# Optimization experiments

Measured on AMD Instinct MI355X. Metric: run time of the kernel, lower is better.

## Reference

```python
import jax, jax.numpy as jnp
import numpy as np

N_HEAD = 16
N_EMBD = 2048
B, S = 2, 2048


def setup_inputs() -> dict:
    key = jax.random.key(0)
    k1, k2, k3 = jax.random.split(key, 3)
    scale = 0.02
    return {
        "hidden_states": jax.random.normal(k1, (B, S, N_EMBD), dtype=jnp.float32),
        "attention_mask": jnp.ones((B, S), dtype=jnp.float32),
        "w_attn": jax.random.normal(k2, (N_EMBD, 3 * N_EMBD), dtype=jnp.float32) * scale,
        "b_attn": jnp.zeros((3 * N_EMBD,), dtype=jnp.float32),
        "w_proj": jax.random.normal(k3, (N_EMBD, N_EMBD), dtype=jnp.float32) * scale,
        "b_proj": jnp.zeros((N_EMBD,), dtype=jnp.float32),
    }


def reference(hidden_states, attention_mask, w_attn, b_attn, w_proj, b_proj):
    b, s, d = hidden_states.shape
    h = N_HEAD
    dh = d // h
    qkv = hidden_states @ w_attn + b_attn          # [b, s, 3d]
    q, k, v = jnp.split(qkv, 3, axis=-1)
    # [b, s, d] -> [b, h, s, dh]
    q = q.reshape(b, s, h, dh).transpose(0, 2, 1, 3)
    k = k.reshape(b, s, h, dh).transpose(0, 2, 1, 3)
    v = v.reshape(b, s, h, dh).transpose(0, 2, 1, 3)
    scores = jnp.einsum("bhqd,bhkd->bhqk", q, k) / jnp.sqrt(jnp.float32(dh))
    # padding mask: [b, s] -> additive bias [b, 1, 1, s]
    bias = (1.0 - attention_mask)[:, None, None, :] * -10000.0
    attn = jax.nn.softmax(scores + bias, axis=-1)   # dropout p=0 (eval)
    out = jnp.einsum("bhqk,bhkd->bhqd", attn, v)    # [b, h, s, dh]
    out = out.transpose(0, 2, 1, 3).reshape(b, s, d)
    return out @ w_proj + b_proj
```

## Files before the change

kernel.cpp:

```cpp
#include <hip/hip_runtime.h>
#include <stdint.h>

#define B_   2
#define S_   2048
#define D_   2048
#define NH_  16
#define DH_  128
#define N3_  6144

typedef unsigned short u16;
typedef __bf16 bf16x8 __attribute__((ext_vector_type(8)));
typedef float  f32x4  __attribute__((ext_vector_type(4)));

#define QSCALE   (0.08838834764831845f * 1.4426950408889634f)
#define BIASF    (-10000.0f * 1.4426950408889634f)

__device__ __forceinline__ u16 f2bf(float f) {
  union { float f; unsigned u; } v; v.f = f;
  unsigned u = v.u;
  return (u16)((u + 0x7FFFu + ((u >> 16) & 1u)) >> 16);
}

__device__ __forceinline__ float fast_exp2(float x) {
  float r;
  asm("v_exp_f32 %0, %1" : "=v"(r) : "v"(x));
  return r;
}

__device__ __forceinline__ unsigned cvtpk(float lo, float hi) {
  unsigned r;
  asm("v_cvt_pk_bf16_f32 %0, %1, %2" : "=v"(r) : "v"(lo), "v"(hi));
  return r;
}

#define GL2LDS(gsrc, ldst)                                                              \
  __builtin_amdgcn_global_load_lds((const __attribute__((address_space(1))) void*)(gsrc), \
      (__attribute__((address_space(3))) void*)(ldst), 16, 0, 0)

__device__ __forceinline__ int swz_id() {
  int id = blockIdx.y * gridDim.x + blockIdx.x;
  int cpx = (gridDim.x * gridDim.y) >> 3;
  return (id & 7) * cpx + (id >> 3);
}

__global__ void cvt_kernel(const float* __restrict__ in, u16* __restrict__ out, int n4) {
  int i = blockIdx.x * blockDim.x + threadIdx.x;
  int stride = gridDim.x * blockDim.x;
  for (; i < n4; i += stride) {
    float4 v = ((const float4*)in)[i];
    ushort4 o;
    o.x = f2bf(v.x); o.y = f2bf(v.y); o.z = f2bf(v.z); o.w = f2bf(v.w);
    ((ushort4*)out)[i] = o;
  }
}

__global__ void transpose_kernel(const float* __restrict__ in, u16* __restrict__ out,
                                 int K, int N) {
  __shared__ float tile[32][33];
  int tx = threadIdx.x, ty = threadIdx.y;
  int nx = blockIdx.x * 32, ky = blockIdx.y * 32;
#pragma unroll
  for (int j = 0; j < 32; j += 8)
    tile[ty + j][tx] = in[(size_t)(ky + ty + j) * N + nx + tx];
  __syncthreads();
#pragma unroll
  for (int j = 0; j < 32; j += 8)
    out[(size_t)(nx + ty + j) * K + ky + tx] = f2bf(tile[tx][ty + j]);
}


#define KS_ABASE(c, h) (lds + (c) * 24576 + (h) * 8192)
#define KS_BBASE(c, h) (lds + (c) * 24576 + 16384 + (h) * 4096)
#define VMCNT(n) asm volatile("s_waitcnt vmcnt(" #n ")" ::: "memory")
#define LGKM0                                            \
  do {                                                   \
    asm volatile("s_waitcnt lgkmcnt(0)" ::: "memory");   \
    __builtin_amdgcn_sched_barrier(0);                   \
  } while (0)
#define BAR __builtin_amdgcn_s_barrier()

__device__ __forceinline__ void ks_read_set(const u16* __restrict__ Ab,
                                            const u16* __restrict__ Bb,
                                            int wrB, int wcB, int lr, int g,
                                            bf16x8 (&af)[4], bf16x8 (&bf)[4]) {
#pragma unroll
  for (int i = 0; i < 4; ++i) {
    int r = wrB + i * 16 + lr;
    int pr = r >> 1;
    int slot = (((r & 1) << 2) | g) ^ (pr & 7);
    af[i] = *reinterpret_cast<const bf16x8*>(Ab + pr * 64 + slot * 8);
  }
#pragma unroll
  for (int j = 0; j < 4; ++j) {
    int n = wcB + j * 16 + lr;
    int pn = n >> 1;
    int slot = (((n & 1) << 2) | g) ^ (pn & 7);
    bf[j] = *reinterpret_cast<const bf16x8*>(Bb + pn * 64 + slot * 8);
  }
}

__device__ __forceinline__ void ks_mfma(const bf16x8 (&af)[4], const bf16x8 (&bf)[4],
                                        f32x4 (&acc)[4][4]) {
  __builtin_amdgcn_s_setprio(1);
#pragma unroll
  for (int i = 0; i < 4; ++i)
#pragma unroll
    for (int j = 0; j < 4; ++j)
      acc[i][j] = __builtin_amdgcn_mfma_f32_16x16x32_bf16(af[i], bf[j], acc[i][j], 0, 0, 0);
  __builtin_amdgcn_s_setprio(0);
}

template <int KD>
__device__ __forceinline__ void ks_stage(const u16* __restrict__ A,
                                         const u16* __restrict__ BT, u16* lds,
                                         int c, int h, int Tg, int m0, int n0, int t) {
#pragma unroll
  for (int inst = 0; inst < 2; ++inst) {
    int idx = inst * 512 + t;
    int pr = idx >> 3, s = idx & 7, v = s ^ (pr & 7);
    int r = pr * 2 + (v >> 2), g = v & 3;
    GL2LDS(A + (size_t)(m0 + r) * KD + Tg * 64 + h * 32 + g * 8,
           KS_ABASE(c, h) + idx * 8);
  }
  {
    int idx = t;
    int pn = idx >> 3, s = idx & 7, v = s ^ (pn & 7);
    int n = pn * 2 + (v >> 2), g = v & 3;
    GL2LDS(BT + (size_t)(n0 + n) * KD + Tg * 64 + h * 32 + g * 8,
           KS_BBASE(c, h) + idx * 8);
  }
}

template <int KD>
__device__ __forceinline__ void gemm_ks_core(const u16* __restrict__ A,
                                             const u16* __restrict__ BT,
                                             int m0, int n0, u16* lds, f32x4 (&acc)[4][4]) {
  const int NT = KD / 64;
  int t = threadIdx.x, wv = t >> 6, lane = t & 63;
  int g = lane >> 4, lr = lane & 15;
  int wrB = (wv >> 1) * 64, wcB = (wv & 1) * 64;
  bf16x8 af0[4], bf0[4], af1[4], bf1[4];

  ks_stage<KD>(A, BT, lds, 0, 0, 0, m0, n0, t);
  ks_stage<KD>(A, BT, lds, 0, 1, 0, m0, n0, t);
  ks_stage<KD>(A, BT, lds, 1, 0, 1, m0, n0, t);
  ks_stage<KD>(A, BT, lds, 1, 1, 1, m0, n0, t);
  VMCNT(6);
  BAR;
  ks_read_set(KS_ABASE(0, 0), KS_BBASE(0, 0), wrB, wcB, lr, g, af0, bf0);
  LGKM0;
  BAR;

  for (int T = 0; T < NT; ++T) {
    int c = T & 1;
    ks_read_set(KS_ABASE(c, 1), KS_BBASE(c, 1), wrB, wcB, lr, g, af1, bf1);
    if (T + 2 < NT) ks_stage<KD>(A, BT, lds, c, 0, T + 2, m0, n0, t);
    BAR;
    LGKM0;
    ks_mfma(af0, bf0, acc);
    BAR;
    if (T + 2 < NT) {
      VMCNT(3);
      ks_stage<KD>(A, BT, lds, c, 1, T + 2, m0, n0, t);
    } else {
      VMCNT(0);
    }
    BAR;
    if (T + 1 < NT)
      ks_read_set(KS_ABASE(c ^ 1, 0), KS_BBASE(c ^ 1, 0), wrB, wcB, lr, g, af0, bf0);
    LGKM0;
    ks_mfma(af1, bf1, acc);
    BAR;
  }
}

__global__ __launch_bounds__(512, 1) void gemm_qkv_kernel(
    const u16* __restrict__ A, const u16* __restrict__ BT, const float* __restrict__ bias,
    u16* __restrict__ Qb, u16* __restrict__ Kb, u16* __restrict__ VTb) {
  __shared__ __attribute__((aligned(16))) u16 lds[49152];
  f32x4 acc[4][4] = {};
  int sw = swz_id();
  int n0 = (sw % gridDim.x) * 128, m0 = (sw / gridDim.x) * 256;
  gemm_ks_core<2048>(A, BT, m0, n0, lds, acc);
  int t = threadIdx.x, lane = t & 63, wv = t >> 6;
  int g = lane >> 4, lr = lane & 15;
  int wrB = (wv >> 1) * 64, wcB = (wv & 1) * 64;
#pragma unroll
  for (int mi = 0; mi < 4; ++mi) {
    int rowbase = m0 + wrB + mi * 16 + g * 4;
    int b = rowbase >> 11, s = rowbase & 2047;
#pragma unroll
    for (int nj = 0; nj < 4; ++nj) {
      int col = n0 + wcB + nj * 16 + lr;
      float bv = bias[col];
      int sec = col >> 11;
      int within = col & 2047;
      int h = within >> 7, d = within & 127;
      if (sec < 2) {
        float mult = (sec == 0) ? QSCALE : 1.0f;
        u16* dst = (sec == 0 ? Qb : Kb) + ((size_t)(b * NH_ + h) * S_ + s) * DH_ + d;
#pragma unroll
        for (int r = 0; r < 4; ++r) dst[(size_t)r * DH_] = f2bf((acc[mi][nj][r] + bv) * mult);
      } else {
        u16* dst = VTb + ((size_t)(b * NH_ + h) * DH_ + d) * S_ + s;
        ushort4 pk;
        pk.x = f2bf(acc[mi][nj][0] + bv); pk.y = f2bf(acc[mi][nj][1] + bv);
        pk.z = f2bf(acc[mi][nj][2] + bv); pk.w = f2bf(acc[mi][nj][3] + bv);
        *reinterpret_cast<ushort4*>(dst) = pk;
      }
    }
  }
}

__global__ __launch_bounds__(512, 1) void gemm_proj_kernel(
    const u16* __restrict__ A, const u16* __restrict__ BT, const float* __restrict__ bias,
    float* __restrict__ out) {
  __shared__ __attribute__((aligned(16))) u16 lds[49152];
  f32x4 acc[4][4] = {};
  int sw = swz_id();
  int n0 = (sw % gridDim.x) * 128, m0 = (sw / gridDim.x) * 256;
  gemm_ks_core<2048>(A, BT, m0, n0, lds, acc);
  int t = threadIdx.x, lane = t & 63, wv = t >> 6;
  int g = lane >> 4, lr = lane & 15;
  int wrB = (wv >> 1) * 64, wcB = (wv & 1) * 64;
#pragma unroll
  for (int mi = 0; mi < 4; ++mi) {
    int rowbase = m0 + wrB + mi * 16 + g * 4;
#pragma unroll
    for (int nj = 0; nj < 4; ++nj) {
      int col = n0 + wcB + nj * 16 + lr;
      float bv = bias[col];
      float* dst = out + (size_t)rowbase * D_ + col;
#pragma unroll
      for (int r = 0; r < 4; ++r) dst[(size_t)r * D_] = acc[mi][nj][r] + bv;
    }
  }
}

__global__ __launch_bounds__(256) void attn_kernel(
    const u16* __restrict__ Qb, const u16* __restrict__ Kb, const u16* __restrict__ VTb,
    const float* __restrict__ mask, u16* __restrict__ AO) {
  __shared__ __attribute__((aligned(16))) u16 Ks[2][64 * 128];
  __shared__ __attribute__((aligned(16))) u16 Vs[2][128 * 64];
  __shared__ float bias_lds[S_];

  int t = threadIdx.x, w = t >> 6, lane = t & 63;
  int g = lane >> 4, lr = lane & 15;
  int sw = swz_id();
  int qt = sw & 31, bh = sw >> 5;
  int b = bh >> 4;
  const u16* Qh = Qb + (size_t)bh * S_ * DH_;
  const u16* Kh = Kb + (size_t)bh * S_ * DH_;
  const u16* Vh = VTb + (size_t)bh * DH_ * S_;
  int q0 = qt * 64 + w * 16;

  for (int i = t; i < S_; i += 256)
    bias_lds[i] = (1.0f - mask[b * S_ + i]) * BIASF;

  bf16x8 bq[4];
#pragma unroll
  for (int kk = 0; kk < 4; ++kk)
    bq[kk] = *reinterpret_cast<const bf16x8*>(Qh + (size_t)(q0 + lr) * DH_ + kk * 32 + g * 8);

  f32x4 oacc[8] = {};
  float m_r = -1e30f, l_r = 0.f;

  __syncthreads();

#define STAGE_KV(buf, s0base)                                                    \
  {                                                                              \
    _Pragma("unroll")                                                            \
    for (int i = 0; i < 4; ++i) {                                                \
      int idx = i * 256 + t;                                                     \
      int row = idx >> 4, slot = idx & 15;                                       \
      GL2LDS(Kh + (size_t)((s0base) + row) * DH_ + ((slot ^ (row & 7)) * 8),     \
             &Ks[buf][idx * 8]);                                                 \
    }                                                                            \
    _Pragma("unroll")                                                            \
    for (int i = 0; i < 4; ++i) {                                                \
      int idx = i * 256 + t;                                                     \
      int row = idx >> 3, slot = idx & 7;                                        \
      GL2LDS(Vh + (size_t)row * S_ + (s0base) + ((slot ^ (row & 7)) * 8),        \
             &Vs[buf][idx * 8]);                                                 \
    }                                                                            \
  }

  STAGE_KV(0, 0);
  const int NT = S_ / 64;
  for (int it = 0; it < NT; ++it) {
    int cur = it & 1;
    if (it + 1 < NT) {
      STAGE_KV(cur ^ 1, (it + 1) * 64);
      asm volatile("s_waitcnt vmcnt(8)" ::: "memory");
    } else {
      asm volatile("s_waitcnt vmcnt(0)" ::: "memory");
    }
    __builtin_amdgcn_s_barrier();
    __builtin_amdgcn_sched_barrier(0);

    f32x4 sacc[4] = {};
    __builtin_amdgcn_s_setprio(1);
#pragma unroll
    for (int kk = 0; kk < 4; ++kk) {
#pragma unroll
      for (int n = 0; n < 4; ++n) {
        int row = lr + 16 * n;
        bf16x8 ak = *reinterpret_cast<const bf16x8*>(
            &Ks[cur][row * 128 + ((((kk << 2) | g) ^ (row & 7)) * 8)]);
        sacc[n] = __builtin_amdgcn_mfma_f32_16x16x32_bf16(ak, bq[kk], sacc[n], 0, 0, 0);
      }
    }
    __builtin_amdgcn_s_setprio(0);

    int s0 = it * 64;
    float sv[4][4];
    float mloc = -3e38f;
#pragma unroll
    for (int n = 0; n < 4; ++n) {
      float4 bb = *reinterpret_cast<const float4*>(&bias_lds[s0 + 16 * n + g * 4]);
      sv[n][0] = sacc[n][0] + bb.x; sv[n][1] = sacc[n][1] + bb.y;
      sv[n][2] = sacc[n][2] + bb.z; sv[n][3] = sacc[n][3] + bb.w;
      mloc = fmaxf(mloc, fmaxf(fmaxf(sv[n][0], sv[n][1]), fmaxf(sv[n][2], sv[n][3])));
    }
    float mx = fmaxf(mloc, __shfl_xor(mloc, 16));
    mx = fmaxf(mx, __shfl_xor(mx, 32));

    if (__any(mx - m_r > 8.f)) {
      float mnew = fmaxf(m_r, mx);
      float f = fast_exp2(m_r - mnew);
      m_r = mnew;
      l_r *= f;
#pragma unroll
      for (int no = 0; no < 8; ++no) oacc[no] *= f;
    }

    unsigned pku[4][2];
#pragma unroll
    for (int n = 0; n < 4; ++n) {
      float p0 = fast_exp2(sv[n][0] - m_r), p1 = fast_exp2(sv[n][1] - m_r);
      float p2 = fast_exp2(sv[n][2] - m_r), p3 = fast_exp2(sv[n][3] - m_r);
      l_r += (p0 + p1) + (p2 + p3);
      pku[n][0] = cvtpk(p0, p1);
      pku[n][1] = cvtpk(p2, p3);
    }

    int srcA = ((g & 1) << 5) + lr;
    int srcB = srcA + 16;
    bool hi = (g >> 1) != 0;
#pragma unroll
    for (int kk2 = 0; kk2 < 2; ++kk2) {
      unsigned a0 = __shfl(pku[2 * kk2][0], srcA), a1 = __shfl(pku[2 * kk2 + 1][0], srcA);
      unsigned b0 = __shfl(pku[2 * kk2][1], srcA), b1 = __shfl(pku[2 * kk2 + 1][1], srcA);
      unsigned c0 = __shfl(pku[2 * kk2][0], srcB), c1 = __shfl(pku[2 * kk2 + 1][0], srcB);
      unsigned d0 = __shfl(pku[2 * kk2][1], srcB), d1 = __shfl(pku[2 * kk2 + 1][1], srcB);
      union { uint4 u; bf16x8 v; } pa;
      pa.u.x = hi ? a1 : a0; pa.u.y = hi ? b1 : b0;
      pa.u.z = hi ? c1 : c0; pa.u.w = hi ? d1 : d0;
      __builtin_amdgcn_s_setprio(1);
#pragma unroll
      for (int no = 0; no < 8; ++no) {
        int d = lr + 16 * no;
        bf16x8 av = *reinterpret_cast<const bf16x8*>(
            &Vs[cur][d * 64 + ((((kk2 << 2) | g) ^ (d & 7)) * 8)]);
        oacc[no] = __builtin_amdgcn_mfma_f32_16x16x32_bf16(av, pa.v, oacc[no], 0, 0, 0);
      }
      __builtin_amdgcn_s_setprio(0);
    }
    __builtin_amdgcn_sched_barrier(0);
    __builtin_amdgcn_s_barrier();
  }
#undef STAGE_KV

  float s = l_r;
  s += __shfl_xor(s, 16);
  s += __shfl_xor(s, 32);
  float inv = 1.0f / s;
  int h = bh & 15;
  int q = q0 + lr;
  u16* dst = AO + ((size_t)(b * S_ + q)) * D_ + h * DH_ + g * 4;
#pragma unroll
  for (int no = 0; no < 8; ++no) {
    ushort4 pk4;
    pk4.x = f2bf(oacc[no][0] * inv); pk4.y = f2bf(oacc[no][1] * inv);
    pk4.z = f2bf(oacc[no][2] * inv); pk4.w = f2bf(oacc[no][3] * inv);
    *reinterpret_cast<ushort4*>(dst + 16 * no) = pk4;
  }
}

extern "C" void kernel_launch(void* const* d_in, const int* in_sizes, int n_in,
                              void* d_out, int out_size, void* d_ws, size_t ws_size,
                              hipStream_t stream) {
  const float* h_in   = (const float*)d_in[0];
  const float* mask   = (const float*)d_in[1];
  const float* w_attn = (const float*)d_in[2];
  const float* b_attn = (const float*)d_in[3];
  const float* w_proj = (const float*)d_in[4];
  const float* b_proj = (const float*)d_in[5];
  float* out = (float*)d_out;

  char* ws = (char*)d_ws;
  u16* Hb  = (u16*)(ws);
  u16* W1T = (u16*)(ws + 16777216);
  u16* W2T = (u16*)(ws + 41943040);
  u16* Qb  = (u16*)(ws + 50331648);
  u16* Kb  = (u16*)(ws + 67108864);
  u16* VTb = (u16*)(ws + 83886080);
  u16* AO  = Hb;

  cvt_kernel<<<2048, 256, 0, stream>>>(h_in, Hb, (B_ * S_ * D_) / 4);
  dim3 tb(32, 8);
  transpose_kernel<<<dim3(N3_ / 32, D_ / 32), tb, 0, stream>>>(w_attn, W1T, D_, N3_);
  transpose_kernel<<<dim3(D_ / 32, D_ / 32), tb, 0, stream>>>(w_proj, W2T, D_, D_);
  gemm_qkv_kernel<<<dim3(N3_ / 128, (B_ * S_) / 256), 512, 0, stream>>>(
      Hb, W1T, b_attn, Qb, Kb, VTb);
  attn_kernel<<<dim3(S_ / 64, B_ * NH_), 256, 0, stream>>>(Qb, Kb, VTb, mask, AO);
  gemm_proj_kernel<<<dim3(D_ / 128, (B_ * S_) / 256), 512, 0, stream>>>(AO, W2T, b_proj, out);
}
```

Measured before the change: 434.7 us.

## Restructure GEMM mainloop into M-quarter staged pipeline with full-K64 LDS tiles

Replaces the K-half split GEMM core with a scheme that stages A in two M-halves and B as full 64-wide K tiles, double-buffered across K steps. Each K step is split into two MFMA phases over M quarters so that the B fragments are reused across both and global-to-LDS loads are interleaved at finer granularity. The goal is better overlap of loads with MFMA and fewer LDS reads of B per step, at the cost of more barriers and a more complex wait-count schedule.

```diff
diff --git a/kernel.cpp b/kernel.cpp
--- a/kernel.cpp
+++ b/kernel.cpp
@@ -69,8 +69,8 @@
 }
 
 
-#define KS_ABASE(c, h) (lds + (c) * 24576 + (h) * 8192)
-#define KS_BBASE(c, h) (lds + (c) * 24576 + 16384 + (h) * 4096)
+#define G8_AB(c, qm) (lds + (c) * 24576 + (qm) * 8192)
+#define G8_BB(c)     (lds + (c) * 24576 + 16384)
 #define VMCNT(n) asm volatile("s_waitcnt vmcnt(" #n ")" ::: "memory")
 #define LGKM0                                            \
   do {                                                   \
@@ -79,99 +79,138 @@
   } while (0)
 #define BAR __builtin_amdgcn_s_barrier()
 
-__device__ __forceinline__ void ks_read_set(const u16* __restrict__ Ab,
-                                            const u16* __restrict__ Bb,
-                                            int wrB, int wcB, int lr, int g,
-                                            bf16x8 (&af)[4], bf16x8 (&bf)[4]) {
-#pragma unroll
-  for (int i = 0; i < 4; ++i) {
-    int r = wrB + i * 16 + lr;
-    int pr = r >> 1;
-    int slot = (((r & 1) << 2) | g) ^ (pr & 7);
-    af[i] = *reinterpret_cast<const bf16x8*>(Ab + pr * 64 + slot * 8);
-  }
-#pragma unroll
-  for (int j = 0; j < 4; ++j) {
-    int n = wcB + j * 16 + lr;
-    int pn = n >> 1;
-    int slot = (((n & 1) << 2) | g) ^ (pn & 7);
-    bf[j] = *reinterpret_cast<const bf16x8*>(Bb + pn * 64 + slot * 8);
-  }
-}
-
-__device__ __forceinline__ void ks_mfma(const bf16x8 (&af)[4], const bf16x8 (&bf)[4],
-                                        f32x4 (&acc)[4][4]) {
-  __builtin_amdgcn_s_setprio(1);
-#pragma unroll
-  for (int i = 0; i < 4; ++i)
-#pragma unroll
-    for (int j = 0; j < 4; ++j)
-      acc[i][j] = __builtin_amdgcn_mfma_f32_16x16x32_bf16(af[i], bf[j], acc[i][j], 0, 0, 0);
-  __builtin_amdgcn_s_setprio(0);
-}
-
 template <int KD>
-__device__ __forceinline__ void ks_stage(const u16* __restrict__ A,
-                                         const u16* __restrict__ BT, u16* lds,
-                                         int c, int h, int Tg, int m0, int n0, int t) {
+__device__ __forceinline__ void stage_ah(const u16* __restrict__ A, u16* lds,
+                                         int k, int qm, int m0, int t) {
+  int c = k & 1;
 #pragma unroll
   for (int inst = 0; inst < 2; ++inst) {
     int idx = inst * 512 + t;
-    int pr = idx >> 3, s = idx & 7, v = s ^ (pr & 7);
-    int r = pr * 2 + (v >> 2), g = v & 3;
-    GL2LDS(A + (size_t)(m0 + r) * KD + Tg * 64 + h * 32 + g * 8,
-           KS_ABASE(c, h) + idx * 8);
-  }
-  {
-    int idx = t;
-    int pn = idx >> 3, s = idx & 7, v = s ^ (pn & 7);
-    int n = pn * 2 + (v >> 2), g = v & 3;
-    GL2LDS(BT + (size_t)(n0 + n) * KD + Tg * 64 + h * 32 + g * 8,
-           KS_BBASE(c, h) + idx * 8);
+    int hr = idx >> 3, p = idx & 7, L = p ^ (hr & 7);
+    int r = ((hr >> 5) << 6) + qm * 32 + (hr & 31);
+    GL2LDS(A + (size_t)(m0 + r) * KD + k * 64 + L * 8,
+           G8_AB(c, qm) + idx * 8);
   }
 }
 
 template <int KD>
-__device__ __forceinline__ void gemm_ks_core(const u16* __restrict__ A,
-                                             const u16* __restrict__ BT,
-                                             int m0, int n0, u16* lds, f32x4 (&acc)[4][4]) {
+__device__ __forceinline__ void stage_bh(const u16* __restrict__ BT, u16* lds,
+                                         int k, int n0, int t) {
+  int c = k & 1;
+#pragma unroll
+  for (int inst = 0; inst < 2; ++inst) {
+    int idx = inst * 512 + t;
+    int hn = idx >> 3, p = idx & 7, L = p ^ (hn & 7);
+    GL2LDS(BT + (size_t)(n0 + hn) * KD + k * 64 + L * 8,
+           G8_BB(c) + idx * 8);
+  }
+}
+
+__device__ __forceinline__ void read_aq(const u16* lds, int c, int qm, int wr, int g,
+                                        int lr, bf16x8 (&af)[2][2]) {
+  const u16* base = G8_AB(c, qm);
+#pragma unroll
+  for (int i = 0; i < 2; ++i) {
+    int hr = wr * 32 + i * 16 + lr;
+#pragma unroll
+    for (int kk = 0; kk < 2; ++kk) {
+      int slot = ((kk << 2) | g) ^ (hr & 7);
+      af[i][kk] = *reinterpret_cast<const bf16x8*>(base + hr * 64 + slot * 8);
+    }
+  }
+}
+
+__device__ __forceinline__ void read_b(const u16* lds, int c, int wc, int g, int lr,
+                                       bf16x8 (&bf)[4][2]) {
+  const u16* base = G8_BB(c);
+#pragma unroll
+  for (int nj = 0; nj < 4; ++nj) {
+    int hn = wc * 64 + nj * 16 + lr;
+#pragma unroll
+    for (int kk = 0; kk < 2; ++kk) {
+      int slot = ((kk << 2) | g) ^ (hn & 7);
+      bf[nj][kk] = *reinterpret_cast<const bf16x8*>(base + hn * 64 + slot * 8);
+    }
+  }
+}
+
+template <int QM>
+__device__ __forceinline__ void mfma_q(const bf16x8 (&af)[2][2], const bf16x8 (&bf)[4][2],
+                                       f32x4 (&acc)[4][4]) {
+  __builtin_amdgcn_s_setprio(1);
+#pragma unroll
+  for (int i = 0; i < 2; ++i)
+#pragma unroll
+    for (int nj = 0; nj < 4; ++nj)
+#pragma unroll
+      for (int kk = 0; kk < 2; ++kk)
+        acc[QM * 2 + i][nj] = __builtin_amdgcn_mfma_f32_16x16x32_bf16(
+            af[i][kk], bf[nj][kk], acc[QM * 2 + i][nj], 0, 0, 0);
+  __builtin_amdgcn_s_setprio(0);
+}
+
+template <int KD>
+__device__ __forceinline__ void gemm8_core(const u16* __restrict__ A,
+                                           const u16* __restrict__ BT,
+                                           int m0, int n0, u16* lds, f32x4 (&acc)[4][4]) {
   const int NT = KD / 64;
+  const int NC = NT / 2;
   int t = threadIdx.x, wv = t >> 6, lane = t & 63;
   int g = lane >> 4, lr = lane & 15;
-  int wrB = (wv >> 1) * 64, wcB = (wv & 1) * 64;
-  bf16x8 af0[4], bf0[4], af1[4], bf1[4];
-
-  ks_stage<KD>(A, BT, lds, 0, 0, 0, m0, n0, t);
-  ks_stage<KD>(A, BT, lds, 0, 1, 0, m0, n0, t);
-  ks_stage<KD>(A, BT, lds, 1, 0, 1, m0, n0, t);
-  ks_stage<KD>(A, BT, lds, 1, 1, 1, m0, n0, t);
-  VMCNT(6);
+  int wr = wv >> 1, wc = wv & 1;
+  bf16x8 af[2][2], bf[4][2];
+
+  stage_ah<KD>(A, lds, 0, 0, m0, t);
+  stage_ah<KD>(A, lds, 0, 1, m0, t);
+  stage_bh<KD>(BT, lds, 0, n0, t);
+  stage_ah<KD>(A, lds, 1, 0, m0, t);
+  stage_ah<KD>(A, lds, 1, 1, m0, t);
+  stage_bh<KD>(BT, lds, 1, n0, t);
+  VMCNT(0);
   BAR;
-  ks_read_set(KS_ABASE(0, 0), KS_BBASE(0, 0), wrB, wcB, lr, g, af0, bf0);
-  LGKM0;
+
+  for (int j = 0; j + 1 < NC; ++j) {
+    read_aq(lds, 0, 0, wr, g, lr, af);
+    read_b(lds, 0, wc, g, lr, bf);
+    if (j >= 1) stage_ah<KD>(A, lds, 2 * j + 1, 1, m0, t);
+    VMCNT(6); BAR; LGKM0;
+    mfma_q<0>(af, bf, acc);
+    BAR;
+    read_aq(lds, 0, 1, wr, g, lr, af);
+    stage_ah<KD>(A, lds, 2 * j + 2, 0, m0, t);
+    stage_bh<KD>(BT, lds, 2 * j + 2, n0, t);
+    VMCNT(6); BAR; LGKM0;
+    mfma_q<1>(af, bf, acc);
+    BAR;
+    read_aq(lds, 1, 0, wr, g, lr, af);
+    read_b(lds, 1, wc, g, lr, bf);
+    stage_ah<KD>(A, lds, 2 * j + 2, 1, m0, t);
+    VMCNT(6); BAR; LGKM0;
+    mfma_q<0>(af, bf, acc);
+    BAR;
+    read_aq(lds, 1, 1, wr, g, lr, af);
+    if (2 * j + 3 < NT) {
+      stage_ah<KD>(A, lds, 2 * j + 3, 0, m0, t);
+      stage_bh<KD>(BT, lds, 2 * j + 3, n0, t);
+    }
+    VMCNT(6); BAR; LGKM0;
+    mfma_q<1>(af, bf, acc);
+    BAR;
+  }
+
+  stage_ah<KD>(A, lds, NT - 1, 1, m0, t);
+  VMCNT(0);
   BAR;
-
-  for (int T = 0; T < NT; ++T) {
-    int c = T & 1;
-    ks_read_set(KS_ABASE(c, 1), KS_BBASE(c, 1), wrB, wcB, lr, g, af1, bf1);
-    if (T + 2 < NT) ks_stage<KD>(A, BT, lds, c, 0, T + 2, m0, n0, t);
-    BAR;
-    LGKM0;
-    ks_mfma(af0, bf0, acc);
-    BAR;
-    if (T + 2 < NT) {
-      VMCNT(3);
-      ks_stage<KD>(A, BT, lds, c, 1, T + 2, m0, n0, t);
-    } else {
-      VMCNT(0);
-    }
-    BAR;
-    if (T + 1 < NT)
-      ks_read_set(KS_ABASE(c ^ 1, 0), KS_BBASE(c ^ 1, 0), wrB, wcB, lr, g, af0, bf0);
-    LGKM0;
-    ks_mfma(af1, bf1, acc);
-    BAR;
-  }
+  read_aq(lds, 0, 0, wr, g, lr, af);
+  read_b(lds, 0, wc, g, lr, bf);
+  mfma_q<0>(af, bf, acc);
+  read_aq(lds, 0, 1, wr, g, lr, af);
+  mfma_q<1>(af, bf, acc);
+  read_aq(lds, 1, 0, wr, g, lr, af);
+  read_b(lds, 1, wc, g, lr, bf);
+  mfma_q<0>(af, bf, acc);
+  read_aq(lds, 1, 1, wr, g, lr, af);
+  mfma_q<1>(af, bf, acc);
 }
 
 __global__ __launch_bounds__(512, 1) void gemm_qkv_kernel(
@@ -181,7 +220,7 @@
   f32x4 acc[4][4] = {};
   int sw = swz_id();
   int n0 = (sw % gridDim.x) * 128, m0 = (sw / gridDim.x) * 256;
-  gemm_ks_core<2048>(A, BT, m0, n0, lds, acc);
+  gemm8_core<2048>(A, BT, m0, n0, lds, acc);
   int t = threadIdx.x, lane = t & 63, wv = t >> 6;
   int g = lane >> 4, lr = lane & 15;
   int wrB = (wv >> 1) * 64, wcB = (wv & 1) * 64;
@@ -219,7 +258,7 @@
   f32x4 acc[4][4] = {};
   int sw = swz_id();
   int n0 = (sw % gridDim.x) * 128, m0 = (sw / gridDim.x) * 256;
-  gemm_ks_core<2048>(A, BT, m0, n0, lds, acc);
+  gemm8_core<2048>(A, BT, m0, n0, lds, acc);
   int t = threadIdx.x, lane = t & 63, wv = t >> 6;
   int g = lane >> 4, lr = lane & 15;
   int wrB = (wv >> 1) * 64, wcB = (wv & 1) * 64;
```

Result: faster. 424.9 us (-2.2%).
